# Kernel optimization log

Measured on AMD Instinct MI355X. Metric: run time of the kernel, lower is better.

Reference implementation:

```python
import jax, jax.numpy as jnp
import numpy as np

ATT_RAW = 312
HID = 900
ATT_DIM = 4096


def setup_inputs() -> dict:
    key = jax.random.key(0)
    ks = jax.random.split(key, 12)
    B, S, N, C = 4, 128, 50, ATT_DIM
    x = jax.random.normal(ks[0], (B, S, C), dtype=jnp.float32)
    x_label = jax.random.randint(ks[1], (B, S), 0, N, dtype=jnp.int64)
    att = jax.random.normal(ks[2], (B, N, ATT_RAW), dtype=jnp.float32)
    att_label = jax.random.randint(ks[3], (B, N), 0, N, dtype=jnp.int64)
    def lin(k, out_f, in_f):
        bound = 1.0 / np.sqrt(in_f)
        kw, kb = jax.random.split(k)
        W = jax.random.uniform(kw, (out_f, in_f), jnp.float32, -bound, bound)
        b = jax.random.uniform(kb, (out_f,), jnp.float32, -bound, bound)
        return W, b
    W1, b1 = lin(ks[4], HID, ATT_RAW)       # attnet layer 1
    W2, b2 = lin(ks[5], ATT_DIM, HID)       # attnet layer 2
    W3, b3 = lin(ks[6], HID, 2 * ATT_DIM)   # o layer 1
    W4, b4 = lin(ks[7], 1, HID)             # o layer 2
    return {"x": x, "x_label": x_label, "att": att, "att_label": att_label,
            "W1": W1, "b1": b1, "W2": W2, "b2": b2,
            "W3": W3, "b3": b3, "W4": W4, "b4": b4}


def reference(x, x_label, att, att_label, W1, b1, W2, b2, W3, b3, W4, b4):
    # x: [B,S,C], att: [B,N,312]; train=True branch -> scalar MSE loss
    B, S, C = x.shape
    N = att.shape[1]
    # attnet: 312 -> 900 -> 4096 with ReLU
    att_f = jax.nn.relu(jax.nn.relu(att @ W1.T + b1) @ W2.T + b2)  # [B,N,4096]
    # o layer 1 on concat([x_f, att_f]) == split matmul + broadcast add
    W3x, W3a = W3[:, :C], W3[:, C:]
    hx = jnp.einsum('bsc,hc->bsh', x, W3x)        # [B,S,900]
    ha = jnp.einsum('bnc,hc->bnh', att_f, W3a)    # [B,N,900]
    pre = jax.nn.relu(hx[:, :, None, :] + ha[:, None, :, :] + b3)  # [B,S,N,900]
    score = jax.nn.sigmoid(jnp.einsum('bsnh,h->bsn', pre, W4[0]) + b4[0])  # [B,S,N]
    label = (x_label[:, :, None] == att_label[:, None, :]).astype(score.dtype)
    loss = jnp.sum((label - score) ** 2) / B / S
    return loss
```

## Files before the change

### kernel.cpp

```cpp
#include <hip/hip_runtime.h>
#include <hip/hip_bf16.h>

typedef __attribute__((ext_vector_type(8))) short bf16x8;
typedef __attribute__((ext_vector_type(4))) float f32x4;
typedef __attribute__((ext_vector_type(8))) unsigned short u16x8;

__device__ __forceinline__ void gload16(const void* g, void* l) {
    __builtin_amdgcn_global_load_lds((const __attribute__((address_space(1))) void*)g,
                                     (__attribute__((address_space(3))) void*)l, 16, 0, 0);
}
__device__ __forceinline__ float bf2f(unsigned short u) {
    union { unsigned i; float f; } v; v.i = ((unsigned)u) << 16; return v.f;
}
__device__ __forceinline__ unsigned short f2bf(float f) {
    __hip_bfloat16 h = __float2bfloat16(f);
    return *(unsigned short*)&h;
}

template<int ROWS>
__device__ __forceinline__ void stage_f32(
    const float* __restrict__ src, int ld, int row0, int rmax,
    int k0, int kmax, short* __restrict__ lds, int tid)
{
    #pragma unroll
    for (int i = 0; i < ROWS / 32; ++i) {
        const int ch = i * 256 + tid;
        const int r = ch >> 3;
        const int kc8 = (ch & 7) * 8;
        const int gr = row0 + r;
        const int gk = k0 + kc8;
        u16x8 v;
        if (gr < rmax && gk + 8 <= kmax) {
            const float* s = src + (size_t)gr * ld + gk;
            const float4 f0 = *(const float4*)s;
            const float4 f1 = *(const float4*)(s + 4);
            const float ff[8] = {f0.x, f0.y, f0.z, f0.w, f1.x, f1.y, f1.z, f1.w};
            #pragma unroll
            for (int j = 0; j < 8; ++j) v[j] = f2bf(ff[j]);
        } else if (gr < rmax && gk < kmax) {
            #pragma unroll
            for (int j = 0; j < 8; ++j) {
                float f = 0.f;
                if (gk + j < kmax) f = src[(size_t)gr * ld + gk + j];
                v[j] = f2bf(f);
            }
        } else {
            v = (u16x8){0, 0, 0, 0, 0, 0, 0, 0};
        }
        *(u16x8*)((char*)lds + r * 128 + ((kc8 * 2) ^ ((r & 7) << 4))) = v;
    }
}

template<int ROWS>
__device__ __forceinline__ void stage_gl(const unsigned short* __restrict__ src,
                                         int ld, int row0, int k0,
                                         short* __restrict__ lds, int w, int l)
{
    const int sr0 = w * 8 + (l >> 3);
    const int scb = (l & 7) * 16;
    #pragma unroll
    for (int c = 0; c < ROWS / 32; ++c) {
        const int r = c * 32 + sr0;
        const int cbs = scb ^ ((r & 7) << 4);
        const char* g = (const char*)(src + (size_t)(row0 + r) * ld + k0) + cbs;
        char* dst = (char*)lds + (size_t)(c * 32 + w * 8) * 128;
        gload16(g, dst);
    }
}

__device__ __forceinline__ void gemm64_body(
    const unsigned short* __restrict__ A, const unsigned short* __restrict__ B,
    const float* __restrict__ bias, unsigned short* __restrict__ Cout, int ldc,
    int bm, int bn, int Kp, int Mtrue,
    short* As, short* Bs, int tid)
{
    const int w = tid >> 6, l = tid & 63;
    const int wm = w >> 1, wn = w & 1;
    f32x4 acc[2][2];
    #pragma unroll
    for (int i = 0; i < 2; ++i)
        #pragma unroll
        for (int j = 0; j < 2; ++j)
            acc[i][j] = (f32x4){0.f, 0.f, 0.f, 0.f};

    for (int k0 = 0; k0 < Kp; k0 += 64) {
        stage_gl<64>(A, Kp, bm, k0, As, w, l);
        stage_gl<64>(B, Kp, bn, k0, Bs, w, l);
        asm volatile("s_waitcnt vmcnt(0)");
        __syncthreads();
        #pragma unroll
        for (int ks = 0; ks < 64; ks += 32) {
            bf16x8 a[2], b[2];
            const int kb = ks * 2 + (l >> 4) * 16;
            #pragma unroll
            for (int i = 0; i < 2; ++i) {
                const int ra = wm * 32 + i * 16 + (l & 15);
                a[i] = *(const bf16x8*)((const char*)As + ra * 128 + (kb ^ ((ra & 7) << 4)));
                const int rb = wn * 32 + i * 16 + (l & 15);
                b[i] = *(const bf16x8*)((const char*)Bs + rb * 128 + (kb ^ ((rb & 7) << 4)));
            }
            #pragma unroll
            for (int i = 0; i < 2; ++i)
                #pragma unroll
                for (int j = 0; j < 2; ++j)
                    acc[i][j] = __builtin_amdgcn_mfma_f32_16x16x32_bf16(a[i], b[j], acc[i][j], 0, 0, 0);
        }
        __syncthreads();
    }

    #pragma unroll
    for (int i = 0; i < 2; ++i) {
        #pragma unroll
        for (int j = 0; j < 2; ++j) {
            const int col = bn + wn * 32 + j * 16 + (l & 15);
            const float bv = bias[col];
            #pragma unroll
            for (int q = 0; q < 4; ++q) {
                const int row = bm + wm * 32 + i * 16 + (l >> 4) * 4 + q;
                float v = fmaxf(acc[i][j][q] + bv, 0.f);
                if (row >= Mtrue) v = 0.f;
                Cout[(size_t)row * ldc + col] = f2bf(v);
            }
        }
    }
}

__device__ __forceinline__ void gemm128_body(
    const unsigned short* __restrict__ A, const unsigned short* __restrict__ B,
    float* __restrict__ slab, int by, int bx, int k_begin, int k_steps, int Mtrue,
    short* As, short* Bs, int tid)
{
    const int w = tid >> 6, l = tid & 63;
    const int wm = w >> 1, wn = w & 1;
    f32x4 acc[4][4];
    #pragma unroll
    for (int i = 0; i < 4; ++i)
        #pragma unroll
        for (int j = 0; j < 4; ++j)
            acc[i][j] = (f32x4){0.f, 0.f, 0.f, 0.f};

    for (int t = 0; t < k_steps; ++t) {
        const int k0 = k_begin + t * 64;
        stage_gl<128>(A, 4096, by * 128, k0, As, w, l);
        stage_gl<128>(B, 4096, bx * 128, k0, Bs, w, l);
        asm volatile("s_waitcnt vmcnt(0)");
        __syncthreads();
        #pragma unroll
        for (int ks = 0; ks < 64; ks += 32) {
            bf16x8 a[4], b[4];
            const int kb = ks * 2 + (l >> 4) * 16;
            #pragma unroll
            for (int i = 0; i < 4; ++i) {
                const int ra = wm * 64 + i * 16 + (l & 15);
                a[i] = *(const bf16x8*)((const char*)As + ra * 128 + (kb ^ ((ra & 7) << 4)));
                const int rb = wn * 64 + i * 16 + (l & 15);
                b[i] = *(const bf16x8*)((const char*)Bs + rb * 128 + (kb ^ ((rb & 7) << 4)));
            }
            #pragma unroll
            for (int i = 0; i < 4; ++i)
                #pragma unroll
                for (int j = 0; j < 4; ++j)
                    acc[i][j] = __builtin_amdgcn_mfma_f32_16x16x32_bf16(a[i], b[j], acc[i][j], 0, 0, 0);
        }
        __syncthreads();
    }

    #pragma unroll
    for (int i = 0; i < 4; ++i) {
        #pragma unroll
        for (int j = 0; j < 4; ++j) {
            const int col = bx * 128 + wn * 64 + j * 16 + (l & 15);
            if (col >= 900) continue;
            #pragma unroll
            for (int q = 0; q < 4; ++q) {
                const int row = by * 128 + wm * 64 + i * 16 + (l >> 4) * 4 + q;
                if (row < Mtrue)
                    slab[(size_t)row * 900 + col] = acc[i][j][q];
            }
        }
    }
}

__device__ __forceinline__ void reduce16(const float* __restrict__ p,
                                         const float* __restrict__ bias,
                                         unsigned short* __restrict__ o,
                                         int M, int idx)
{
    const int m = idx / 113;
    const int c = idx - m * 113;
    const int k = c * 8;
    u16x8 v;
    #pragma unroll
    for (int q = 0; q < 8; q += 4) {
        if (k + q < 900) {
            float4 a = *(const float4*)(p + (size_t)m * 900 + k + q);
            #pragma unroll 1
            for (int s = 1; s < 16; ++s) {
                const float4 t = *(const float4*)(p + ((size_t)s * M + m) * 900 + k + q);
                a.x += t.x; a.y += t.y; a.z += t.z; a.w += t.w;
            }
            if (bias) {
                const float4 bb = *(const float4*)(bias + k + q);
                a.x += bb.x; a.y += bb.y; a.z += bb.z; a.w += bb.w;
            }
            v[q + 0] = f2bf(a.x); v[q + 1] = f2bf(a.y);
            v[q + 2] = f2bf(a.z); v[q + 3] = f2bf(a.w);
        } else {
            #pragma unroll
            for (int j = 0; j < 4; ++j) v[q + j] = 0;
        }
    }
    *(u16x8*)(o + (size_t)m * 904 + k) = v;
}

struct PadJob {
    const float* src; unsigned short* dst;
    int src_ld, col0, M, K, Kp;
    int chunk_begin;
};
struct PG1Args {
    PadJob j[4]; int total;
    const float *att, *W1, *b1;
    unsigned short* h1;
};

__global__ __launch_bounds__(256)
void padg1(PG1Args P)
{
    __shared__ short As[64 * 64];
    __shared__ short Bs[64 * 64];
    const int gid = blockIdx.x;
    const int tid = threadIdx.x;

    if (gid < 60) {
        const int bm = (gid & 3) * 64, bn = (gid >> 2) * 64;
        const int w = tid >> 6, l = tid & 63;
        const int wm = w >> 1, wn = w & 1;

        f32x4 acc[2][2];
        #pragma unroll
        for (int i = 0; i < 2; ++i)
            #pragma unroll
            for (int j = 0; j < 2; ++j)
                acc[i][j] = (f32x4){0.f, 0.f, 0.f, 0.f};

        for (int k0 = 0; k0 < 320; k0 += 64) {
            stage_f32<64>(P.att, 312, bm, 200, k0, 312, As, tid);
            stage_f32<64>(P.W1,  312, bn, 900, k0, 312, Bs, tid);
            __syncthreads();
            #pragma unroll
            for (int ks = 0; ks < 64; ks += 32) {
                bf16x8 a[2], b[2];
                const int kb = ks * 2 + (l >> 4) * 16;
                #pragma unroll
                for (int i = 0; i < 2; ++i) {
                    const int ra = wm * 32 + i * 16 + (l & 15);
                    a[i] = *(const bf16x8*)((const char*)As + ra * 128 + (kb ^ ((ra & 7) << 4)));
                    const int rb = wn * 32 + i * 16 + (l & 15);
                    b[i] = *(const bf16x8*)((const char*)Bs + rb * 128 + (kb ^ ((rb & 7) << 4)));
                }
                #pragma unroll
                for (int i = 0; i < 2; ++i)
                    #pragma unroll
                    for (int j = 0; j < 2; ++j)
                        acc[i][j] = __builtin_amdgcn_mfma_f32_16x16x32_bf16(a[i], b[j], acc[i][j], 0, 0, 0);
            }
            __syncthreads();
        }

        #pragma unroll
        for (int i = 0; i < 2; ++i) {
            #pragma unroll
            for (int j = 0; j < 2; ++j) {
                const int col = bn + wn * 32 + j * 16 + (l & 15);
                const float bv = (col < 900) ? P.b1[col] : 0.f;
                #pragma unroll
                for (int q = 0; q < 4; ++q) {
                    const int row = bm + wm * 32 + i * 16 + (l >> 4) * 4 + q;
                    float v = fmaxf(acc[i][j][q] + bv, 0.f);
                    if (row >= 200) v = 0.f;
                    P.h1[(size_t)row * 960 + col] = f2bf(v);
                }
            }
        }
        return;
    }

    const int idx = (gid - 60) * 256 + tid;
    if (idx >= P.total) return;
    int ji = 0;
    #pragma unroll
    for (int k = 1; k < 4; ++k) if (idx >= P.j[k].chunk_begin) ji = k;
    const PadJob J = P.j[ji];
    const int cid = idx - J.chunk_begin;
    const int kp8 = J.Kp >> 3;
    const int m = cid / kp8;
    const int kc = (cid - m * kp8) << 3;
    u16x8 v;
    if (m < J.M && kc + 8 <= J.K) {
        const float* s = J.src + (size_t)m * J.src_ld + J.col0 + kc;
        const float4 f0 = *(const float4*)s;
        const float4 f1 = *(const float4*)(s + 4);
        const float ff[8] = {f0.x, f0.y, f0.z, f0.w, f1.x, f1.y, f1.z, f1.w};
        #pragma unroll
        for (int j = 0; j < 8; ++j) v[j] = f2bf(ff[j]);
    } else {
        #pragma unroll
        for (int j = 0; j < 8; ++j) {
            float f = 0.f;
            const int k = kc + j;
            if (m < J.M && k < J.K) f = J.src[(size_t)m * J.src_ld + J.col0 + k];
            v[j] = f2bf(f);
        }
    }
    *(u16x8*)(J.dst + (size_t)m * J.Kp + kc) = v;
}

struct G23Args {
    const unsigned short *h1, *W2; const float* b2; unsigned short* attf;
    const unsigned short *xb, *W3x; float* hxp;
};

__global__ __launch_bounds__(256)
void g2g3(G23Args a)
{
    __shared__ short As[128 * 64];
    __shared__ short Bs[128 * 64];
    const int gid = blockIdx.x;
    const int tid = threadIdx.x;

    if (gid < 256) {
        const int bm = (gid >> 6) * 64, bn = (gid & 63) * 64;
        gemm64_body(a.h1, a.W2, a.b2, a.attf, 4096, bm, bn, 960, 200, As, Bs, tid);
    } else {
        const int g3 = gid - 256;
        const int z = g3 >> 5, by = (g3 >> 3) & 3, bx = g3 & 7;
        gemm128_body(a.xb, a.W3x, a.hxp + (size_t)z * 512 * 900,
                     by, bx, z * 256, 4, 512, As, Bs, tid);
    }
}

struct G4RArgs {
    const unsigned short *attf, *W3a; float* hap;
    const float *hxp, *b3; unsigned short* hx_bf;
};

__global__ __launch_bounds__(256)
void g4redhx(G4RArgs a)
{
    __shared__ short As[128 * 64];
    __shared__ short Bs[128 * 64];
    const int gid = blockIdx.x;
    const int tid = threadIdx.x;

    if (gid < 256) {
        const int z = gid >> 4, by = (gid >> 3) & 1, bx = gid & 7;
        gemm128_body(a.attf, a.W3a, a.hap + (size_t)z * 200 * 900,
                     by, bx, z * 256, 4, 200, As, Bs, tid);
    } else {
        const int idx = (gid - 256) * 256 + tid;
        reduce16(a.hxp, a.b3, a.hx_bf, 512, idx);
    }
}

__global__ __launch_bounds__(256)
void reduce_ha(const float* __restrict__ hap, unsigned short* __restrict__ ha_bf)
{
    const int idx = blockIdx.x * 256 + threadIdx.x;
    if (idx >= 200 * 113) return;
    reduce16(hap, nullptr, ha_bf, 200, idx);
}

__global__ __launch_bounds__(512)
void score_loss(const unsigned short* __restrict__ hxb,
                const unsigned short* __restrict__ hab,
                const float* __restrict__ W4,
                const float* __restrict__ b4,
                const int* __restrict__ xl,
                const int* __restrict__ al,
                float* __restrict__ part)
{
    __shared__ __align__(16) unsigned short hxs[8 * 904];
    __shared__ __align__(16) unsigned short has[16 * 904];
    __shared__ __align__(16) float w4s[904];
    __shared__ float zpart[4][8][16];
    __shared__ float red[2];

    const int tid = threadIdx.x;
    const int nt = blockIdx.x, st = blockIdx.y, b = blockIdx.z;
    const int row0 = b * 128 + st * 8;

    for (int t = tid; t < 24 * 113; t += 512) {
        u16x8 v;
        unsigned short* dst;
        if (t < 8 * 113) {
            const int r = t / 113, c = t - r * 113;
            v = *(const u16x8*)(hxb + (size_t)(row0 + r) * 904 + c * 8);
            dst = hxs + r * 904 + c * 8;
        } else {
            const int t2 = t - 8 * 113;
            const int r = t2 / 113, c = t2 - r * 113;
            const int n = nt * 16 + r;
            if (n < 50) v = *(const u16x8*)(hab + (size_t)(b * 50 + n) * 904 + c * 8);
            else        v = (u16x8){0,0,0,0,0,0,0,0};
            dst = has + r * 904 + c * 8;
        }
        *(u16x8*)dst = v;
    }
    for (int t = tid; t < 226; t += 512) {
        float4 v = {0.f, 0.f, 0.f, 0.f};
        if (t < 225) v = *(const float4*)(W4 + t * 4);
        *(float4*)(w4s + t * 4) = v;
    }
    __syncthreads();

    const int hs = tid >> 7;
    const int si = (tid >> 4) & 7;
    const int ni = tid & 15;

    float acc = 0.f;
    const unsigned short* hrow = hxs + si * 904;
    const unsigned short* arow = has + ni * 904;
    for (int c = hs; c < 113; c += 4) {
        const u16x8 hv = *(const u16x8*)(hrow + c * 8);
        const u16x8 av = *(const u16x8*)(arow + c * 8);
        const float4 w0 = *(const float4*)(w4s + c * 8);
        const float4 w1 = *(const float4*)(w4s + c * 8 + 4);
        const float ww[8] = {w0.x, w0.y, w0.z, w0.w, w1.x, w1.y, w1.z, w1.w};
        #pragma unroll
        for (int j = 0; j < 8; ++j) {
            const float u = bf2f((unsigned short)hv[j]) + bf2f((unsigned short)av[j]);
            acc = fmaf(fmaxf(u, 0.f), ww[j], acc);
        }
    }
    zpart[hs][si][ni] = acc;
    __syncthreads();

    float dd = 0.f;
    if (tid < 128) {
        const int esi = tid >> 4, eni = tid & 15;
        const int n = nt * 16 + eni;
        const float z = zpart[0][esi][eni] + zpart[1][esi][eni]
                      + zpart[2][esi][eni] + zpart[3][esi][eni] + b4[0];
        const float sc = 1.f / (1.f + __expf(-z));
        if (n < 50) {
            const float lab = (xl[row0 + esi] == al[b * 50 + n]) ? 1.f : 0.f;
            const float d = lab - sc;
            dd = d * d;
        }
        #pragma unroll
        for (int off = 32; off > 0; off >>= 1)
            dd += __shfl_down(dd, off);
        if ((tid & 63) == 0) red[tid >> 6] = dd;
    }
    __syncthreads();
    if (tid == 0)
        part[nt + 4 * (st + 16 * b)] = red[0] + red[1];
}

__global__ __launch_bounds__(256)
void final_loss(const float* __restrict__ part, float* __restrict__ out)
{
    __shared__ float r[4];
    const int tid = threadIdx.x;
    float v = part[tid];
    #pragma unroll
    for (int off = 32; off > 0; off >>= 1)
        v += __shfl_down(v, off);
    if ((tid & 63) == 0) r[tid >> 6] = v;
    __syncthreads();
    if (tid == 0) out[0] = (r[0] + r[1] + r[2] + r[3]) * (1.f / 512.f);
}

extern "C" void kernel_launch(void* const* d_in, const int* in_sizes, int n_in,
                              void* d_out, int out_size, void* d_ws, size_t ws_size,
                              hipStream_t stream)
{
    const float* x   = (const float*)d_in[0];
    const int*   xl  = (const int*)  d_in[1];
    const float* att = (const float*)d_in[2];
    const int*   al  = (const int*)  d_in[3];
    const float* W1  = (const float*)d_in[4];
    const float* b1  = (const float*)d_in[5];
    const float* W2  = (const float*)d_in[6];
    const float* b2  = (const float*)d_in[7];
    const float* W3  = (const float*)d_in[8];
    const float* b3  = (const float*)d_in[9];
    const float* W4  = (const float*)d_in[10];
    const float* b4  = (const float*)d_in[11];
    float* out = (float*)d_out;

    const int B = 4, S = 128, N = 50, C = 4096, H = 900, AR = 312;
    const int MS = B * S;
    const int MN = B * N;
    const int MNp = 256;
    const int Hp = 960;
    const int W3p = 1024;
    const int SPL = 16;

    char* base = (char*)d_ws;
    size_t off = 0;
    auto alloc = [&](size_t bytes) { void* r = base + off; off = (off + bytes + 255) & ~(size_t)255; return r; };
    unsigned short* x_bf   = (unsigned short*)alloc((size_t)MS * C * 2);
    unsigned short* W2_bf  = (unsigned short*)alloc((size_t)C * Hp * 2);
    unsigned short* W3x_bf = (unsigned short*)alloc((size_t)W3p * C * 2);
    unsigned short* W3a_bf = (unsigned short*)alloc((size_t)W3p * C * 2);
    unsigned short* h1_bf  = (unsigned short*)alloc((size_t)MNp * Hp * 2);
    unsigned short* attf_bf= (unsigned short*)alloc((size_t)MNp * C * 2);
    float* hxp = (float*)alloc((size_t)SPL * MS * H * 4);
    float* hap = (float*)alloc((size_t)SPL * MN * H * 4);
    unsigned short* hx_bf = (unsigned short*)alloc((size_t)MS * 904 * 2);
    unsigned short* ha_bf = (unsigned short*)alloc((size_t)MN * 904 * 2);
    float* part = (float*)alloc(256 * 4);

    const dim3 blk(256);
    auto cdiv = [](int a, int b) { return (a + b - 1) / b; };

    PG1Args P;
    int cb = 0;
    auto setjob = [&](int i, const float* src, unsigned short* dst, int ld, int col0,
                      int M, int K, int Kp, int Mp) {
        P.j[i] = PadJob{src, dst, ld, col0, M, K, Kp, cb};
        cb += Mp * (Kp >> 3);
    };
    setjob(0, x,   x_bf,   C,     0, MS, C,  C,   MS);
    setjob(1, W2,  W2_bf,  H,     0, C,  H,  Hp,  C);
    setjob(2, W3,  W3x_bf, 2 * C, 0, H,  C,  C,   W3p);
    setjob(3, W3,  W3a_bf, 2 * C, C, H,  C,  C,   W3p);
    P.total = cb;
    P.att = att; P.W1 = W1; P.b1 = b1; P.h1 = h1_bf;
    padg1<<<dim3(60 + cdiv(cb, 256)), blk, 0, stream>>>(P);

    G23Args a23{h1_bf, W2_bf, b2, attf_bf, x_bf, W3x_bf, hxp};
    g2g3<<<dim3(768), blk, 0, stream>>>(a23);

    G4RArgs a4r{attf_bf, W3a_bf, hap, hxp, b3, hx_bf};
    g4redhx<<<dim3(482), blk, 0, stream>>>(a4r);

    reduce_ha<<<dim3(cdiv(MN * 113, 256)), blk, 0, stream>>>(hap, ha_bf);

    score_loss<<<dim3(4, 16, 4), dim3(512), 0, stream>>>(hx_bf, ha_bf, W4, b4, xl, al, part);
    final_loss<<<dim3(1), blk, 0, stream>>>(part, out);
}
```

Before: 75.10 us.

## Replace split-K partial slabs and reduce kernels with atomic accumulation

```diff
diff --git a/kernel.cpp b/kernel.cpp
--- a/kernel.cpp
+++ b/kernel.cpp
@@ -15,6 +15,33 @@
 __device__ __forceinline__ unsigned short f2bf(float f) {
     __hip_bfloat16 h = __float2bfloat16(f);
     return *(unsigned short*)&h;
+}
+
+__device__ __forceinline__ void conv_chunk(
+    const float* __restrict__ src, int ld, int col0, int M, int K, int Kp,
+    unsigned short* __restrict__ dst, int cid)
+{
+    const int kp8 = Kp >> 3;
+    const int m = cid / kp8;
+    const int kc = (cid - m * kp8) << 3;
+    u16x8 v;
+    if (m < M && kc + 8 <= K) {
+        const float* s = src + (size_t)m * ld + col0 + kc;
+        const float4 f0 = *(const float4*)s;
+        const float4 f1 = *(const float4*)(s + 4);
+        const float ff[8] = {f0.x, f0.y, f0.z, f0.w, f1.x, f1.y, f1.z, f1.w};
+        #pragma unroll
+        for (int j = 0; j < 8; ++j) v[j] = f2bf(ff[j]);
+    } else {
+        #pragma unroll
+        for (int j = 0; j < 8; ++j) {
+            float f = 0.f;
+            const int k = kc + j;
+            if (m < M && k < K) f = src[(size_t)m * ld + col0 + k];
+            v[j] = f2bf(f);
+        }
+    }
+    *(u16x8*)(dst + (size_t)m * Kp + kc) = v;
 }
 
 template<int ROWS>
@@ -125,9 +152,9 @@
     }
 }
 
-__device__ __forceinline__ void gemm128_body(
+__device__ __forceinline__ void gemm128_atomic(
     const unsigned short* __restrict__ A, const unsigned short* __restrict__ B,
-    float* __restrict__ slab, int by, int bx, int k_begin, int k_steps, int Mtrue,
+    float* __restrict__ dstf, int by, int bx, int k_begin, int k_steps, int Mtrue,
     short* As, short* Bs, int tid)
 {
     const int w = tid >> 6, l = tid & 63;
@@ -175,57 +202,22 @@
             for (int q = 0; q < 4; ++q) {
                 const int row = by * 128 + wm * 64 + i * 16 + (l >> 4) * 4 + q;
                 if (row < Mtrue)
-                    slab[(size_t)row * 900 + col] = acc[i][j][q];
-            }
-        }
-    }
-}
-
-__device__ __forceinline__ void reduce16(const float* __restrict__ p,
-                                         const float* __restrict__ bias,
-                                         unsigned short* __restrict__ o,
-                                         int M, int idx)
-{
-    const int m = idx / 113;
-    const int c = idx - m * 113;
-    const int k = c * 8;
-    u16x8 v;
-    #pragma unroll
-    for (int q = 0; q < 8; q += 4) {
-        if (k + q < 900) {
-            float4 a = *(const float4*)(p + (size_t)m * 900 + k + q);
-            #pragma unroll 1
-            for (int s = 1; s < 16; ++s) {
-                const float4 t = *(const float4*)(p + ((size_t)s * M + m) * 900 + k + q);
-                a.x += t.x; a.y += t.y; a.z += t.z; a.w += t.w;
-            }
-            if (bias) {
-                const float4 bb = *(const float4*)(bias + k + q);
-                a.x += bb.x; a.y += bb.y; a.z += bb.z; a.w += bb.w;
-            }
-            v[q + 0] = f2bf(a.x); v[q + 1] = f2bf(a.y);
-            v[q + 2] = f2bf(a.z); v[q + 3] = f2bf(a.w);
-        } else {
-            #pragma unroll
-            for (int j = 0; j < 4; ++j) v[q + j] = 0;
-        }
-    }
-    *(u16x8*)(o + (size_t)m * 904 + k) = v;
-}
-
-struct PadJob {
-    const float* src; unsigned short* dst;
-    int src_ld, col0, M, K, Kp;
-    int chunk_begin;
+                    unsafeAtomicAdd(&dstf[(size_t)row * 904 + col], acc[i][j][q]);
+            }
+        }
+    }
+}
+
+struct L1Args {
+    const float *att, *W1, *b1; unsigned short* h1;
+    const float* x;  unsigned short* x_bf;
+    const float* W2; unsigned short* W2_bf;
+    const float* W3; unsigned short* W3x_bf;
+    const float* b3; float *hx, *ha;
 };
-struct PG1Args {
-    PadJob j[4]; int total;
-    const float *att, *W1, *b1;
-    unsigned short* h1;
-};
 
 __global__ __launch_bounds__(256)
-void padg1(PG1Args P)
+void padg1(L1Args P)
 {
     __shared__ short As[64 * 64];
     __shared__ short Bs[64 * 64];
@@ -286,43 +278,48 @@
         return;
     }
 
-    const int idx = (gid - 60) * 256 + tid;
-    if (idx >= P.total) return;
-    int ji = 0;
-    #pragma unroll
-    for (int k = 1; k < 4; ++k) if (idx >= P.j[k].chunk_begin) ji = k;
-    const PadJob J = P.j[ji];
-    const int cid = idx - J.chunk_begin;
-    const int kp8 = J.Kp >> 3;
-    const int m = cid / kp8;
-    const int kc = (cid - m * kp8) << 3;
-    u16x8 v;
-    if (m < J.M && kc + 8 <= J.K) {
-        const float* s = J.src + (size_t)m * J.src_ld + J.col0 + kc;
-        const float4 f0 = *(const float4*)s;
-        const float4 f1 = *(const float4*)(s + 4);
-        const float ff[8] = {f0.x, f0.y, f0.z, f0.w, f1.x, f1.y, f1.z, f1.w};
-        #pragma unroll
-        for (int j = 0; j < 8; ++j) v[j] = f2bf(ff[j]);
+    if (gid < 1084) {
+        conv_chunk(P.x, 4096, 0, 512, 4096, 4096, P.x_bf, (gid - 60) * 256 + tid);
+        return;
+    }
+    if (gid < 3004) {
+        conv_chunk(P.W2, 900, 0, 4096, 900, 960, P.W2_bf, (gid - 1084) * 256 + tid);
+        return;
+    }
+    if (gid < 5052) {
+        conv_chunk(P.W3, 8192, 0, 900, 4096, 4096, P.W3x_bf, (gid - 3004) * 256 + tid);
+        return;
+    }
+    int idx = (gid - 5052) * 256 + tid;
+    if (idx < 57856) {
+        const int m = idx / 113;
+        const int c = idx - m * 113;
+        const int k = c * 8;
+        float f[8];
+        #pragma unroll
+        for (int j = 0; j < 8; ++j) f[j] = (k + j < 900) ? P.b3[k + j] : 0.f;
+        float* d = P.hx + (size_t)m * 904 + k;
+        *(float4*)d       = (float4){f[0], f[1], f[2], f[3]};
+        *(float4*)(d + 4) = (float4){f[4], f[5], f[6], f[7]};
     } else {
-        #pragma unroll
-        for (int j = 0; j < 8; ++j) {
-            float f = 0.f;
-            const int k = kc + j;
-            if (m < J.M && k < J.K) f = J.src[(size_t)m * J.src_ld + J.col0 + k];
-            v[j] = f2bf(f);
-        }
-    }
-    *(u16x8*)(J.dst + (size_t)m * J.Kp + kc) = v;
-}
-
-struct G23Args {
-    const unsigned short *h1, *W2; const float* b2; unsigned short* attf;
-    const unsigned short *xb, *W3x; float* hxp;
+        idx -= 57856;
+        if (idx >= 22600) return;
+        const int m = idx / 113;
+        const int c = idx - m * 113;
+        float* d = P.ha + (size_t)m * 904 + c * 8;
+        *(float4*)d       = (float4){0.f, 0.f, 0.f, 0.f};
+        *(float4*)(d + 4) = (float4){0.f, 0.f, 0.f, 0.f};
+    }
+}
+
+struct L2Args {
+    const unsigned short *h1, *W2b; const float* b2; unsigned short* attf;
+    const unsigned short *xb, *W3xb; float* hx;
+    const float* W3; unsigned short* W3a_bf;
 };
 
 __global__ __launch_bounds__(256)
-void g2g3(G23Args a)
+void g2g3w(L2Args a)
 {
     __shared__ short As[128 * 64];
     __shared__ short Bs[128 * 64];
@@ -331,54 +328,40 @@
 
     if (gid < 256) {
         const int bm = (gid >> 6) * 64, bn = (gid & 63) * 64;
-        gemm64_body(a.h1, a.W2, a.b2, a.attf, 4096, bm, bn, 960, 200, As, Bs, tid);
+        gemm64_body(a.h1, a.W2b, a.b2, a.attf, 4096, bm, bn, 960, 200, As, Bs, tid);
+    } else if (gid < 768) {
+        const int g = gid - 256;
+        const int z = g >> 5, by = (g >> 3) & 3, bx = g & 7;
+        gemm128_atomic(a.xb, a.W3xb, a.hx, by, bx, z * 256, 4, 512, As, Bs, tid);
     } else {
-        const int g3 = gid - 256;
-        const int z = g3 >> 5, by = (g3 >> 3) & 3, bx = g3 & 7;
-        gemm128_body(a.xb, a.W3x, a.hxp + (size_t)z * 512 * 900,
-                     by, bx, z * 256, 4, 512, As, Bs, tid);
-    }
-}
-
-struct G4RArgs {
-    const unsigned short *attf, *W3a; float* hap;
-    const float *hxp, *b3; unsigned short* hx_bf;
+        conv_chunk(a.W3, 8192, 4096, 900, 4096, 4096, a.W3a_bf, (gid - 768) * 256 + tid);
+    }
+}
+
+struct L3Args {
+    const unsigned short *attf, *W3ab; float* ha; float* out;
 };
 
 __global__ __launch_bounds__(256)
-void g4redhx(G4RArgs a)
+void g4z(L3Args a)
 {
     __shared__ short As[128 * 64];
     __shared__ short Bs[128 * 64];
     const int gid = blockIdx.x;
     const int tid = threadIdx.x;
-
-    if (gid < 256) {
-        const int z = gid >> 4, by = (gid >> 3) & 1, bx = gid & 7;
-        gemm128_body(a.attf, a.W3a, a.hap + (size_t)z * 200 * 900,
-                     by, bx, z * 256, 4, 200, As, Bs, tid);
-    } else {
-        const int idx = (gid - 256) * 256 + tid;
-        reduce16(a.hxp, a.b3, a.hx_bf, 512, idx);
-    }
-}
-
-__global__ __launch_bounds__(256)
-void reduce_ha(const float* __restrict__ hap, unsigned short* __restrict__ ha_bf)
-{
-    const int idx = blockIdx.x * 256 + threadIdx.x;
-    if (idx >= 200 * 113) return;
-    reduce16(hap, nullptr, ha_bf, 200, idx);
+    if (gid == 0 && tid == 0) a.out[0] = 0.f;
+    const int z = gid >> 4, by = (gid >> 3) & 1, bx = gid & 7;
+    gemm128_atomic(a.attf, a.W3ab, a.ha, by, bx, z * 256, 4, 200, As, Bs, tid);
 }
 
 __global__ __launch_bounds__(512)
-void score_loss(const unsigned short* __restrict__ hxb,
-                const unsigned short* __restrict__ hab,
+void score_loss(const float* __restrict__ hx,
+                const float* __restrict__ ha,
                 const float* __restrict__ W4,
                 const float* __restrict__ b4,
                 const int* __restrict__ xl,
                 const int* __restrict__ al,
-                float* __restrict__ part)
+                float* __restrict__ out)
 {
     __shared__ __align__(16) unsigned short hxs[8 * 904];
     __shared__ __align__(16) unsigned short has[16 * 904];
@@ -391,20 +374,32 @@
     const int row0 = b * 128 + st * 8;
 
     for (int t = tid; t < 24 * 113; t += 512) {
-        u16x8 v;
+        float f[8] = {0.f, 0.f, 0.f, 0.f, 0.f, 0.f, 0.f, 0.f};
         unsigned short* dst;
         if (t < 8 * 113) {
             const int r = t / 113, c = t - r * 113;
-            v = *(const u16x8*)(hxb + (size_t)(row0 + r) * 904 + c * 8);
+            const float* p = hx + (size_t)(row0 + r) * 904 + c * 8;
+            const float4 a0 = *(const float4*)p;
+            const float4 a1 = *(const float4*)(p + 4);
+            f[0] = a0.x; f[1] = a0.y; f[2] = a0.z; f[3] = a0.w;
+            f[4] = a1.x; f[5] = a1.y; f[6] = a1.z; f[7] = a1.w;
             dst = hxs + r * 904 + c * 8;
         } else {
             const int t2 = t - 8 * 113;
             const int r = t2 / 113, c = t2 - r * 113;
             const int n = nt * 16 + r;
-            if (n < 50) v = *(const u16x8*)(hab + (size_t)(b * 50 + n) * 904 + c * 8);
-            else        v = (u16x8){0,0,0,0,0,0,0,0};
+            if (n < 50) {
+                const float* p = ha + (size_t)(b * 50 + n) * 904 + c * 8;
+                const float4 a0 = *(const float4*)p;
+                const float4 a1 = *(const float4*)(p + 4);
+                f[0] = a0.x; f[1] = a0.y; f[2] = a0.z; f[3] = a0.w;
+                f[4] = a1.x; f[5] = a1.y; f[6] = a1.z; f[7] = a1.w;
+            }
             dst = has + r * 904 + c * 8;
         }
+        u16x8 v;
+        #pragma unroll
+        for (int j = 0; j < 8; ++j) v[j] = f2bf(f[j]);
         *(u16x8*)dst = v;
     }
     for (int t = tid; t < 226; t += 512) {
@@ -455,21 +450,7 @@
     }
     __syncthreads();
     if (tid == 0)
-        part[nt + 4 * (st + 16 * b)] = red[0] + red[1];
-}
-
-__global__ __launch_bounds__(256)
-void final_loss(const float* __restrict__ part, float* __restrict__ out)
-{
-    __shared__ float r[4];
-    const int tid = threadIdx.x;
-    float v = part[tid];
-    #pragma unroll
-    for (int off = 32; off > 0; off >>= 1)
-        v += __shfl_down(v, off);
-    if ((tid & 63) == 0) r[tid >> 6] = v;
-    __syncthreads();
-    if (tid == 0) out[0] = (r[0] + r[1] + r[2] + r[3]) * (1.f / 512.f);
+        atomicAdd(out, (red[0] + red[1]) * (1.f / 512.f));
 }
 
 extern "C" void kernel_launch(void* const* d_in, const int* in_sizes, int n_in,
@@ -490,13 +471,7 @@
     const float* b4  = (const float*)d_in[11];
     float* out = (float*)d_out;
 
-    const int B = 4, S = 128, N = 50, C = 4096, H = 900, AR = 312;
-    const int MS = B * S;
-    const int MN = B * N;
-    const int MNp = 256;
-    const int Hp = 960;
-    const int W3p = 1024;
-    const int SPL = 16;
+    const int MS = 512, C = 4096, Hp = 960, MNp = 256, W3p = 1024;
 
     char* base = (char*)d_ws;
     size_t off = 0;
@@ -507,38 +482,19 @@
     unsigned short* W3a_bf = (unsigned short*)alloc((size_t)W3p * C * 2);
     unsigned short* h1_bf  = (unsigned short*)alloc((size_t)MNp * Hp * 2);
     unsigned short* attf_bf= (unsigned short*)alloc((size_t)MNp * C * 2);
-    float* hxp = (float*)alloc((size_t)SPL * MS * H * 4);
-    float* hap = (float*)alloc((size_t)SPL * MN * H * 4);
-    unsigned short* hx_bf = (unsigned short*)alloc((size_t)MS * 904 * 2);
-    unsigned short* ha_bf = (unsigned short*)alloc((size_t)MN * 904 * 2);
-    float* part = (float*)alloc(256 * 4);
+    float* hx = (float*)alloc((size_t)512 * 904 * 4);
+    float* ha = (float*)alloc((size_t)200 * 904 * 4);
 
     const dim3 blk(256);
-    auto cdiv = [](int a, int b) { return (a + b - 1) / b; };
-
-    PG1Args P;
-    int cb = 0;
-    auto setjob = [&](int i, const float* src, unsigned short* dst, int ld, int col0,
-                      int M, int K, int Kp, int Mp) {
-        P.j[i] = PadJob{src, dst, ld, col0, M, K, Kp, cb};
-        cb += Mp * (Kp >> 3);
-    };
-    setjob(0, x,   x_bf,   C,     0, MS, C,  C,   MS);
-    setjob(1, W2,  W2_bf,  H,     0, C,  H,  Hp,  C);
-    setjob(2, W3,  W3x_bf, 2 * C, 0, H,  C,  C,   W3p);
-    setjob(3, W3,  W3a_bf, 2 * C, C, H,  C,  C,   W3p);
-    P.total = cb;
-    P.att = att; P.W1 = W1; P.b1 = b1; P.h1 = h1_bf;
-    padg1<<<dim3(60 + cdiv(cb, 256)), blk, 0, stream>>>(P);
-
-    G23Args a23{h1_bf, W2_bf, b2, attf_bf, x_bf, W3x_bf, hxp};
-    g2g3<<<dim3(768), blk, 0, stream>>>(a23);
-
-    G4RArgs a4r{attf_bf, W3a_bf, hap, hxp, b3, hx_bf};
-    g4redhx<<<dim3(482), blk, 0, stream>>>(a4r);
-
-    reduce_ha<<<dim3(cdiv(MN * 113, 256)), blk, 0, stream>>>(hap, ha_bf);
-
-    score_loss<<<dim3(4, 16, 4), dim3(512), 0, stream>>>(hx_bf, ha_bf, W4, b4, xl, al, part);
-    final_loss<<<dim3(1), blk, 0, stream>>>(part, out);
-}
+
+    L1Args P{att, W1, b1, h1_bf, x, x_bf, W2, W2_bf, W3, W3x_bf, b3, hx, ha};
+    padg1<<<dim3(5367), blk, 0, stream>>>(P);
+
+    L2Args A2{h1_bf, W2_bf, b2, attf_bf, x_bf, W3x_bf, hx, W3, W3a_bf};
+    g2g3w<<<dim3(2816), blk, 0, stream>>>(A2);
+
+    L3Args A3{attf_bf, W3a_bf, ha, out};
+    g4z<<<dim3(256), blk, 0, stream>>>(A3);
+
+    score_loss<<<dim3(4, 16, 4), dim3(512), 0, stream>>>(hx, ha, W4, b4, xl, al, out);
+}
```

After: 100.3 us. 33.5% more time.

## Rebalance kernel stages: defer W3a conversion, halve hx split-K, atomic loss

Applied to the files above, without the earlier changes.

```diff
diff --git a/kernel.cpp b/kernel.cpp
--- a/kernel.cpp
+++ b/kernel.cpp
@@ -15,6 +15,33 @@
 __device__ __forceinline__ unsigned short f2bf(float f) {
     __hip_bfloat16 h = __float2bfloat16(f);
     return *(unsigned short*)&h;
+}
+
+__device__ __forceinline__ void conv_chunk(
+    const float* __restrict__ src, int ld, int col0, int M, int K, int Kp,
+    unsigned short* __restrict__ dst, int cid)
+{
+    const int kp8 = Kp >> 3;
+    const int m = cid / kp8;
+    const int kc = (cid - m * kp8) << 3;
+    u16x8 v;
+    if (m < M && kc + 8 <= K) {
+        const float* s = src + (size_t)m * ld + col0 + kc;
+        const float4 f0 = *(const float4*)s;
+        const float4 f1 = *(const float4*)(s + 4);
+        const float ff[8] = {f0.x, f0.y, f0.z, f0.w, f1.x, f1.y, f1.z, f1.w};
+        #pragma unroll
+        for (int j = 0; j < 8; ++j) v[j] = f2bf(ff[j]);
+    } else {
+        #pragma unroll
+        for (int j = 0; j < 8; ++j) {
+            float f = 0.f;
+            const int k = kc + j;
+            if (m < M && k < K) f = src[(size_t)m * ld + col0 + k];
+            v[j] = f2bf(f);
+        }
+    }
+    *(u16x8*)(dst + (size_t)m * Kp + kc) = v;
 }
 
 template<int ROWS>
@@ -181,7 +208,8 @@
     }
 }
 
-__device__ __forceinline__ void reduce16(const float* __restrict__ p,
+template<int NS>
+__device__ __forceinline__ void reduceNS(const float* __restrict__ p,
                                          const float* __restrict__ bias,
                                          unsigned short* __restrict__ o,
                                          int M, int idx)
@@ -195,7 +223,7 @@
         if (k + q < 900) {
             float4 a = *(const float4*)(p + (size_t)m * 900 + k + q);
             #pragma unroll 1
-            for (int s = 1; s < 16; ++s) {
+            for (int s = 1; s < NS; ++s) {
                 const float4 t = *(const float4*)(p + ((size_t)s * M + m) * 900 + k + q);
                 a.x += t.x; a.y += t.y; a.z += t.z; a.w += t.w;
             }
@@ -219,9 +247,10 @@
     int chunk_begin;
 };
 struct PG1Args {
-    PadJob j[4]; int total;
+    PadJob j[3]; int total;
     const float *att, *W1, *b1;
     unsigned short* h1;
+    float* out;
 };
 
 __global__ __launch_bounds__(256)
@@ -286,43 +315,25 @@
         return;
     }
 
+    if (gid == 60 && tid == 0) P.out[0] = 0.f;
+
     const int idx = (gid - 60) * 256 + tid;
     if (idx >= P.total) return;
     int ji = 0;
     #pragma unroll
-    for (int k = 1; k < 4; ++k) if (idx >= P.j[k].chunk_begin) ji = k;
+    for (int k = 1; k < 3; ++k) if (idx >= P.j[k].chunk_begin) ji = k;
     const PadJob J = P.j[ji];
-    const int cid = idx - J.chunk_begin;
-    const int kp8 = J.Kp >> 3;
-    const int m = cid / kp8;
-    const int kc = (cid - m * kp8) << 3;
-    u16x8 v;
-    if (m < J.M && kc + 8 <= J.K) {
-        const float* s = J.src + (size_t)m * J.src_ld + J.col0 + kc;
-        const float4 f0 = *(const float4*)s;
-        const float4 f1 = *(const float4*)(s + 4);
-        const float ff[8] = {f0.x, f0.y, f0.z, f0.w, f1.x, f1.y, f1.z, f1.w};
-        #pragma unroll
-        for (int j = 0; j < 8; ++j) v[j] = f2bf(ff[j]);
-    } else {
-        #pragma unroll
-        for (int j = 0; j < 8; ++j) {
-            float f = 0.f;
-            const int k = kc + j;
-            if (m < J.M && k < J.K) f = J.src[(size_t)m * J.src_ld + J.col0 + k];
-            v[j] = f2bf(f);
-        }
-    }
-    *(u16x8*)(J.dst + (size_t)m * J.Kp + kc) = v;
-}
-
-struct G23Args {
-    const unsigned short *h1, *W2; const float* b2; unsigned short* attf;
-    const unsigned short *xb, *W3x; float* hxp;
+    conv_chunk(J.src, J.src_ld, J.col0, J.M, J.K, J.Kp, J.dst, idx - J.chunk_begin);
+}
+
+struct L2Args {
+    const unsigned short *xb, *W3xb; float* hxp;
+    const unsigned short *h1, *W2b; const float* b2; unsigned short* attf;
+    const float* W3; unsigned short* W3a_bf;
 };
 
 __global__ __launch_bounds__(256)
-void g2g3(G23Args a)
+void g23w(L2Args a)
 {
     __shared__ short As[128 * 64];
     __shared__ short Bs[128 * 64];
@@ -330,23 +341,25 @@
     const int tid = threadIdx.x;
 
     if (gid < 256) {
-        const int bm = (gid >> 6) * 64, bn = (gid & 63) * 64;
-        gemm64_body(a.h1, a.W2, a.b2, a.attf, 4096, bm, bn, 960, 200, As, Bs, tid);
+        const int z = gid >> 5, by = (gid >> 3) & 3, bx = gid & 7;
+        gemm128_body(a.xb, a.W3xb, a.hxp + (size_t)z * 512 * 900,
+                     by, bx, z * 512, 8, 512, As, Bs, tid);
+    } else if (gid < 512) {
+        const int g = gid - 256;
+        gemm64_body(a.h1, a.W2b, a.b2, a.attf, 4096,
+                    (g >> 6) * 64, (g & 63) * 64, 960, 200, As, Bs, tid);
     } else {
-        const int g3 = gid - 256;
-        const int z = g3 >> 5, by = (g3 >> 3) & 3, bx = g3 & 7;
-        gemm128_body(a.xb, a.W3x, a.hxp + (size_t)z * 512 * 900,
-                     by, bx, z * 256, 4, 512, As, Bs, tid);
-    }
-}
-
-struct G4RArgs {
-    const unsigned short *attf, *W3a; float* hap;
+        conv_chunk(a.W3, 8192, 4096, 900, 4096, 4096, a.W3a_bf, (gid - 512) * 256 + tid);
+    }
+}
+
+struct L3Args {
+    const unsigned short *attf, *W3ab; float* hap;
     const float *hxp, *b3; unsigned short* hx_bf;
 };
 
 __global__ __launch_bounds__(256)
-void g4redhx(G4RArgs a)
+void g4r(L3Args a)
 {
     __shared__ short As[128 * 64];
     __shared__ short Bs[128 * 64];
@@ -355,20 +368,19 @@
 
     if (gid < 256) {
         const int z = gid >> 4, by = (gid >> 3) & 1, bx = gid & 7;
-        gemm128_body(a.attf, a.W3a, a.hap + (size_t)z * 200 * 900,
+        gemm128_body(a.attf, a.W3ab, a.hap + (size_t)z * 200 * 900,
                      by, bx, z * 256, 4, 200, As, Bs, tid);
     } else {
         const int idx = (gid - 256) * 256 + tid;
-        reduce16(a.hxp, a.b3, a.hx_bf, 512, idx);
+        if (idx < 57856) reduceNS<8>(a.hxp, a.b3, a.hx_bf, 512, idx);
     }
 }
 
 __global__ __launch_bounds__(256)
-void reduce_ha(const float* __restrict__ hap, unsigned short* __restrict__ ha_bf)
+void red_ha(const float* __restrict__ hap, unsigned short* __restrict__ ha_bf)
 {
     const int idx = blockIdx.x * 256 + threadIdx.x;
-    if (idx >= 200 * 113) return;
-    reduce16(hap, nullptr, ha_bf, 200, idx);
+    if (idx < 22600) reduceNS<16>(hap, nullptr, ha_bf, 200, idx);
 }
 
 __global__ __launch_bounds__(512)
@@ -378,7 +390,7 @@
                 const float* __restrict__ b4,
                 const int* __restrict__ xl,
                 const int* __restrict__ al,
-                float* __restrict__ part)
+                float* __restrict__ out)
 {
     __shared__ __align__(16) unsigned short hxs[8 * 904];
     __shared__ __align__(16) unsigned short has[16 * 904];
@@ -455,21 +467,7 @@
     }
     __syncthreads();
     if (tid == 0)
-        part[nt + 4 * (st + 16 * b)] = red[0] + red[1];
-}
-
-__global__ __launch_bounds__(256)
-void final_loss(const float* __restrict__ part, float* __restrict__ out)
-{
-    __shared__ float r[4];
-    const int tid = threadIdx.x;
-    float v = part[tid];
-    #pragma unroll
-    for (int off = 32; off > 0; off >>= 1)
-        v += __shfl_down(v, off);
-    if ((tid & 63) == 0) r[tid >> 6] = v;
-    __syncthreads();
-    if (tid == 0) out[0] = (r[0] + r[1] + r[2] + r[3]) * (1.f / 512.f);
+        atomicAdd(out, (red[0] + red[1]) * (1.f / 512.f));
 }
 
 extern "C" void kernel_launch(void* const* d_in, const int* in_sizes, int n_in,
@@ -496,7 +494,6 @@
     const int MNp = 256;
     const int Hp = 960;
     const int W3p = 1024;
-    const int SPL = 16;
 
     char* base = (char*)d_ws;
     size_t off = 0;
@@ -507,11 +504,10 @@
     unsigned short* W3a_bf = (unsigned short*)alloc((size_t)W3p * C * 2);
     unsigned short* h1_bf  = (unsigned short*)alloc((size_t)MNp * Hp * 2);
     unsigned short* attf_bf= (unsigned short*)alloc((size_t)MNp * C * 2);
-    float* hxp = (float*)alloc((size_t)SPL * MS * H * 4);
-    float* hap = (float*)alloc((size_t)SPL * MN * H * 4);
+    float* hxp = (float*)alloc((size_t)8 * MS * H * 4);
+    float* hap = (float*)alloc((size_t)16 * MN * H * 4);
     unsigned short* hx_bf = (unsigned short*)alloc((size_t)MS * 904 * 2);
     unsigned short* ha_bf = (unsigned short*)alloc((size_t)MN * 904 * 2);
-    float* part = (float*)alloc(256 * 4);
 
     const dim3 blk(256);
     auto cdiv = [](int a, int b) { return (a + b - 1) / b; };
@@ -526,19 +522,17 @@
     setjob(0, x,   x_bf,   C,     0, MS, C,  C,   MS);
     setjob(1, W2,  W2_bf,  H,     0, C,  H,  Hp,  C);
     setjob(2, W3,  W3x_bf, 2 * C, 0, H,  C,  C,   W3p);
-    setjob(3, W3,  W3a_bf, 2 * C, C, H,  C,  C,   W3p);
     P.total = cb;
-    P.att = att; P.W1 = W1; P.b1 = b1; P.h1 = h1_bf;
+    P.att = att; P.W1 = W1; P.b1 = b1; P.h1 = h1_bf; P.out = out;
     padg1<<<dim3(60 + cdiv(cb, 256)), blk, 0, stream>>>(P);
 
-    G23Args a23{h1_bf, W2_bf, b2, attf_bf, x_bf, W3x_bf, hxp};
-    g2g3<<<dim3(768), blk, 0, stream>>>(a23);
-
-    G4RArgs a4r{attf_bf, W3a_bf, hap, hxp, b3, hx_bf};
-    g4redhx<<<dim3(482), blk, 0, stream>>>(a4r);
-
-    reduce_ha<<<dim3(cdiv(MN * 113, 256)), blk, 0, stream>>>(hap, ha_bf);
-
-    score_loss<<<dim3(4, 16, 4), dim3(512), 0, stream>>>(hx_bf, ha_bf, W4, b4, xl, al, part);
-    final_loss<<<dim3(1), blk, 0, stream>>>(part, out);
-}
+    L2Args A2{x_bf, W3x_bf, hxp, h1_bf, W2_bf, b2, attf_bf, W3, W3a_bf};
+    g23w<<<dim3(2560), blk, 0, stream>>>(A2);
+
+    L3Args A3{attf_bf, W3a_bf, hap, hxp, b3, hx_bf};
+    g4r<<<dim3(482), blk, 0, stream>>>(A3);
+
+    red_ha<<<dim3(cdiv(MN * 113, 256)), blk, 0, stream>>>(hap, ha_bf);
+
+    score_loss<<<dim3(4, 16, 4), dim3(512), 0, stream>>>(hx_bf, ha_bf, W4, b4, xl, al, out);
+}
```

New measurement: 70.38 us. -6.3%, faster.
